# Kernel optimization log

Measured on AMD Instinct MI355X. Metric: run time of the kernel, lower is better.

The kernel has to match this reference:

```python
import jax, jax.numpy as jnp
import numpy as np

TOP_K = 2

def _expert(x, w1, w2, w3):
    return (jax.nn.silu(x @ w1.T) * (x @ w3.T)) @ w2.T

def setup_inputs() -> dict:
    key = jax.random.key(0)
    ks = jax.random.split(key, 8)
    B, L, D, F, E, S = 4, 2048, 1024, 512, 16, 1
    p = lambda k, shape: (jax.random.normal(k, shape, jnp.float32) * 0.02)
    return {
        "x": jax.random.normal(ks[0], (B, L, D), jnp.float32),
        "gate_w": p(ks[1], (E, D)),
        "expert_bias": jnp.zeros((E,), jnp.float32),
        "sw1": p(ks[2], (S, F, D)),
        "sw2": p(ks[3], (S, D, F)),
        "sw3": p(ks[4], (S, F, D)),
        "ew1": p(ks[5], (E, F, D)),
        "ew2": p(ks[6], (E, D, F)),
        "ew3": p(ks[7], (E, F, D)),
    }

def reference(x, gate_w, expert_bias, sw1, sw2, sw3, ew1, ew2, ew3):
    B, L, D = x.shape
    E = gate_w.shape[0]
    flat_x = x.reshape(-1, D)  # [T, D], T = B*L

    # Shared experts (always-on)
    shared = sum(_expert(flat_x, sw1[i], sw2[i], sw3[i]) for i in range(sw1.shape[0]))

    # Router (eval mode: no jitter noise, no bias update; expert_bias buffer added)
    logits = flat_x @ gate_w.T + expert_bias          # [T, E]
    probs = jax.nn.softmax(logits, axis=-1)
    topw, topi = jax.lax.top_k(probs, TOP_K)          # [T, k]
    topw = topw / jnp.sum(topw, axis=-1, keepdims=True)

    # Routed experts: combine weight per (token, expert); zero weight => zero contribution,
    # identical math to the masked gather/scatter in the original.
    out = jnp.zeros_like(flat_x)
    for e in range(E):  # fixed small structural loop over experts
        cw = jnp.sum(jnp.where(topi == e, topw, 0.0), axis=-1)  # [T]
        out = out + cw[:, None] * _expert(flat_x, ew1[e], ew2[e], ew3[e])

    y = (shared + out).reshape(B, L, D)
    return y, probs
```

## Files before the change

### kernel.cpp

```cpp
#include <hip/hip_runtime.h>

typedef unsigned short u16;
typedef __bf16 bf16_t;
typedef bf16_t bf16x8 __attribute__((ext_vector_type(8)));
typedef float f32x4 __attribute__((ext_vector_type(4)));

#define T_TOK 8192
#define DIM   1024
#define FF    512
#define NE    16
#define RBASE_SHARED (2 * T_TOK)
#define NROWS (RBASE_SHARED + T_TOK)
#define MAXTILES 256
#define NSEG 512

__device__ __forceinline__ u16 f2bf(float f) {
  union { float f; unsigned u; } v; v.f = f;
  unsigned r = v.u + 0x7FFFu + ((v.u >> 16) & 1u);
  return (u16)(r >> 16);
}
__device__ __forceinline__ float bf2f(u16 h) {
  union { unsigned u; float f; } v; v.u = ((unsigned)h) << 16; return v.f;
}
__device__ __forceinline__ int clampi(int v, int lo, int hi) {
  return v < lo ? lo : (v > hi ? hi : v);
}

#define GLL16(g, l) __builtin_amdgcn_global_load_lds( \
    (const __attribute__((address_space(1))) void*)(g), \
    (__attribute__((address_space(3))) void*)(l), 16, 0, 0)

#define WAIT_VM_BARRIER(n) asm volatile("s_waitcnt vmcnt(" #n ")\n\ts_barrier" ::: "memory")
#define WAIT_LGKM0()       asm volatile("s_waitcnt lgkmcnt(0)" ::: "memory")

#define SW4  131072
#define EW4  2097152
#define TOTW4 (3 * SW4 + 3 * EW4)

__global__ __launch_bounds__(256) void cvt_all_kernel(
    const float* __restrict__ sw1, const float* __restrict__ sw2,
    const float* __restrict__ sw3, const float* __restrict__ ew1,
    const float* __restrict__ ew2, const float* __restrict__ ew3,
    u16* __restrict__ sw1b, u16* __restrict__ sw2b, u16* __restrict__ sw3b,
    u16* __restrict__ ew1b, u16* __restrict__ ew2b, u16* __restrict__ ew3b) {
  int i = blockIdx.x * 256 + threadIdx.x;
  const float* s; u16* dst; int j;
  if (i < SW4)                      { s = sw1; dst = sw1b; j = i; }
  else if (i < 2 * SW4)             { s = sw2; dst = sw2b; j = i - SW4; }
  else if (i < 3 * SW4)             { s = sw3; dst = sw3b; j = i - 2 * SW4; }
  else if (i < 3 * SW4 + EW4)       { s = ew1; dst = ew1b; j = i - 3 * SW4; }
  else if (i < 3 * SW4 + 2 * EW4)   { s = ew2; dst = ew2b; j = i - (3 * SW4 + EW4); }
  else if (i < TOTW4)               { s = ew3; dst = ew3b; j = i - (3 * SW4 + 2 * EW4); }
  else return;
  float4 v = reinterpret_cast<const float4*>(s)[j];
  ushort4 o;
  o.x = f2bf(v.x); o.y = f2bf(v.y); o.z = f2bf(v.z); o.w = f2bf(v.w);
  reinterpret_cast<ushort4*>(dst)[j] = o;
}

__global__ __launch_bounds__(256) void router_kernel(
    const float* __restrict__ x, const float* __restrict__ gw,
    const float* __restrict__ ebias, float* __restrict__ probs,
    int* __restrict__ topi, float* __restrict__ topw, int* __restrict__ cnt_seg,
    u16* __restrict__ xb) {
  __shared__ int hist[16];
  int tid = threadIdx.x;
  int lane = tid & 63, w = tid >> 6;
  if (tid < 16) hist[tid] = 0;
  __syncthreads();
  const float4* gv = reinterpret_cast<const float4*>(gw);
  for (int it = 0; it < 2; ++it) {
    int t0 = blockIdx.x * 16 + (w + 4 * it) * 2;
    const float4* x0 = reinterpret_cast<const float4*>(x + (size_t)t0 * DIM);
    const float4* x1 = reinterpret_cast<const float4*>(x + (size_t)(t0 + 1) * DIM);
    float4 xa[4], xc[4];
#pragma unroll
    for (int j = 0; j < 4; ++j) { xa[j] = x0[j * 64 + lane]; xc[j] = x1[j * 64 + lane]; }
    u16* xr0 = xb + (size_t)t0 * DIM;
    u16* xr1 = xb + (size_t)(t0 + 1) * DIM;
#pragma unroll
    for (int j = 0; j < 4; ++j) {
      ushort4 o0, o1;
      o0.x = f2bf(xa[j].x); o0.y = f2bf(xa[j].y); o0.z = f2bf(xa[j].z); o0.w = f2bf(xa[j].w);
      o1.x = f2bf(xc[j].x); o1.y = f2bf(xc[j].y); o1.z = f2bf(xc[j].z); o1.w = f2bf(xc[j].w);
      reinterpret_cast<ushort4*>(xr0)[j * 64 + lane] = o0;
      reinterpret_cast<ushort4*>(xr1)[j * 64 + lane] = o1;
    }
    float p0[16], p1[16];
#pragma unroll
    for (int e = 0; e < NE; ++e) {
      float s0 = 0.f, s1 = 0.f;
#pragma unroll
      for (int j = 0; j < 4; ++j) {
        float4 g = gv[e * 256 + j * 64 + lane];
        s0 += xa[j].x * g.x + xa[j].y * g.y + xa[j].z * g.z + xa[j].w * g.w;
        s1 += xc[j].x * g.x + xc[j].y * g.y + xc[j].z * g.z + xc[j].w * g.w;
      }
#pragma unroll
      for (int d = 1; d < 64; d <<= 1) { s0 += __shfl_xor(s0, d); s1 += __shfl_xor(s1, d); }
      float b = ebias[e];
      p0[e] = s0 + b; p1[e] = s1 + b;
    }
    float m0 = p0[0], m1 = p1[0];
#pragma unroll
    for (int e = 1; e < NE; ++e) { m0 = fmaxf(m0, p0[e]); m1 = fmaxf(m1, p1[e]); }
    float sum0 = 0.f, sum1 = 0.f;
#pragma unroll
    for (int e = 0; e < NE; ++e) {
      p0[e] = __expf(p0[e] - m0); sum0 += p0[e];
      p1[e] = __expf(p1[e] - m1); sum1 += p1[e];
    }
    float inv0 = 1.f / sum0, inv1 = 1.f / sum1;
#pragma unroll
    for (int e = 0; e < NE; ++e) { p0[e] *= inv0; p1[e] *= inv1; }
    if (lane == 0) {
#pragma unroll
      for (int j = 0; j < 4; ++j)
        reinterpret_cast<float4*>(probs + (size_t)t0 * NE)[j] =
            make_float4(p0[4 * j], p0[4 * j + 1], p0[4 * j + 2], p0[4 * j + 3]);
      float b1 = -1.f, b2 = -1.f; int i1 = 0, i2 = 0;
#pragma unroll
      for (int e = 0; e < NE; ++e) {
        float pe = p0[e];
        if (pe > b1) { b2 = b1; i2 = i1; b1 = pe; i1 = e; }
        else if (pe > b2) { b2 = pe; i2 = e; }
      }
      float ws = b1 + b2;
      reinterpret_cast<int2*>(topi)[t0] = make_int2(i1, i2);
      reinterpret_cast<float2*>(topw)[t0] = make_float2(b1 / ws, b2 / ws);
      atomicAdd(&hist[i1], 1); atomicAdd(&hist[i2], 1);
    }
    if (lane == 1) {
      int t1 = t0 + 1;
#pragma unroll
      for (int j = 0; j < 4; ++j)
        reinterpret_cast<float4*>(probs + (size_t)t1 * NE)[j] =
            make_float4(p1[4 * j], p1[4 * j + 1], p1[4 * j + 2], p1[4 * j + 3]);
      float b1 = -1.f, b2 = -1.f; int i1 = 0, i2 = 0;
#pragma unroll
      for (int e = 0; e < NE; ++e) {
        float pe = p1[e];
        if (pe > b1) { b2 = b1; i2 = i1; b1 = pe; i1 = e; }
        else if (pe > b2) { b2 = pe; i2 = e; }
      }
      float ws = b1 + b2;
      reinterpret_cast<int2*>(topi)[t1] = make_int2(i1, i2);
      reinterpret_cast<float2*>(topw)[t1] = make_float2(b1 / ws, b2 / ws);
      atomicAdd(&hist[i1], 1); atomicAdd(&hist[i2], 1);
    }
  }
  __syncthreads();
  if (tid < 16) cnt_seg[blockIdx.x * 16 + tid] = hist[tid];
}

__global__ __launch_bounds__(256) void scan_kernel(
    const int* __restrict__ cnt_seg, int* __restrict__ cnt, int* __restrict__ offs,
    int* __restrict__ seg_base, int2* __restrict__ tab) {
  __shared__ int chunk_sum[16][16];
  __shared__ int chunk_base[16][16];
  __shared__ int tot[16], off_s[17];
  int tid = threadIdx.x;
  int e = tid & 15, c = tid >> 4;
  int s0 = 0;
  for (int s = 0; s < 32; ++s) s0 += cnt_seg[(c * 32 + s) * 16 + e];
  chunk_sum[c][e] = s0;
  __syncthreads();
  if (tid < 16) {
    int r = 0;
    for (int c2 = 0; c2 < 16; ++c2) { chunk_base[c2][tid] = r; r += chunk_sum[c2][tid]; }
    tot[tid] = r;
  }
  __syncthreads();
  if (tid == 0) {
    int a = 0;
    for (int i = 0; i < 16; ++i) { off_s[i] = a; offs[i] = a; cnt[i] = tot[i]; a += tot[i]; }
    off_s[16] = RBASE_SHARED; offs[16] = RBASE_SHARED;
    for (int i = 0; i < MAXTILES; ++i) tab[i] = make_int2(-1, 0);
    int loadc[8]  = {0, 0, 0, 0, 0, 0, 0, 0};
    int cursor[8] = {0, 0, 0, 0, 0, 0, 0, 0};
    for (int g = 0; g < 16; ++g) {
      int nt = (tot[g] + 127) >> 7;
      if (nt == 0) continue;
      int best = 0;
      for (int c2 = 1; c2 < 8; ++c2) if (loadc[c2] < loadc[best]) best = c2;
      loadc[best] += nt;
      int c2 = best;
      for (int ti = 0; ti < nt; ++ti) {
        while (cursor[c2] >= 32) c2 = (c2 + 1) & 7;
        tab[c2 * 32 + cursor[c2]] = make_int2(g, ti * 128);
        cursor[c2]++;
      }
    }
    for (int ti = 0; ti < 64; ++ti) {
      int c2 = ti & 7;
      while (cursor[c2] >= 32) c2 = (c2 + 1) & 7;
      tab[c2 * 32 + cursor[c2]] = make_int2(16, ti * 128);
      cursor[c2]++;
    }
  }
  __syncthreads();
  int r = off_s[e] + chunk_base[c][e];
  for (int s = 0; s < 32; ++s) {
    int seg = c * 32 + s;
    seg_base[seg * 16 + e] = r;
    r += cnt_seg[seg * 16 + e];
  }
}

__global__ __launch_bounds__(64) void scatter_kernel(
    const int* __restrict__ topi, const float* __restrict__ topw,
    const int* __restrict__ seg_base,
    int* __restrict__ idx, float* __restrict__ cwl, int* __restrict__ slotmap) {
  __shared__ int ti[16][2]; __shared__ float tw[16][2]; __shared__ int base[16];
  int b = blockIdx.x;
  int tid = threadIdx.x;
  if (tid < 16) {
    int t = b * 16 + tid;
    int2 pp = reinterpret_cast<const int2*>(topi)[t];
    ti[tid][0] = clampi(pp.x, 0, 15); ti[tid][1] = clampi(pp.y, 0, 15);
    float2 ww = reinterpret_cast<const float2*>(topw)[t];
    tw[tid][0] = ww.x; tw[tid][1] = ww.y;
    base[tid] = seg_base[b * 16 + tid];
  }
  __syncthreads();
  if (tid < 32) {
    int l = tid >> 1, s = tid & 1;
    int t = b * 16 + l;
    int e = ti[l][s];
    int rank = 0;
    for (int t2 = 0; t2 < 16; ++t2) {
      if (ti[t2][0] == e && (t2 < l || (t2 == l && 0 < s))) ++rank;
      if (ti[t2][1] == e && (t2 < l)) ++rank;
    }
    int slot = clampi(base[e] + rank, 0, NROWS - 1);
    idx[slot] = t; cwl[slot] = tw[l][s]; slotmap[t * 3 + s] = slot;
  } else if (tid < 48) {
    int l = tid - 32;
    int t = b * 16 + l;
    int sh = RBASE_SHARED + t;
    idx[sh] = t; cwl[sh] = 1.0f; slotmap[t * 3 + 2] = sh;
  }
}

__global__ __launch_bounds__(256, 2) void gemm_silu_kernel(
    const u16* __restrict__ A, const u16* __restrict__ sw1b, const u16* __restrict__ sw3b,
    const u16* __restrict__ ew1b, const u16* __restrict__ ew3b, u16* __restrict__ G,
    const int2* __restrict__ tab, const int* __restrict__ offs,
    const int* __restrict__ cnt, const int* __restrict__ gidx) {
  const int K = DIM;
  int orig = blockIdx.x;
  int xcd = orig & 7;
  int u = orig >> 3;
  int tslot = u >> 2, ny = u & 3;
  int tileid = xcd * 32 + tslot;
  int2 te = tab[tileid];
  int e = te.x;
  if (e < 0) return;
  e = clampi(e, 0, NE);
  int m0 = te.y;
  int M = (e == NE) ? T_TOK : cnt[e];
  M = clampi(M, 1, T_TOK);
  int rowbase = clampi(offs[e], 0, NROWS - 1);
  const u16* B1 = (e == NE) ? sw1b : ew1b + (size_t)e * FF * K;
  const u16* B3 = (e == NE) ? sw3b : ew3b + (size_t)e * FF * K;
  int n0 = ny * 128;

  __shared__ u16 As[3 * 4096], B1s[3 * 4096], B3s[3 * 4096];

  int tid = threadIdx.x;
  int lane = tid & 63, wv = tid >> 6;
  int srow = tid >> 2, sg = tid & 3;
  int sk0 = (sg ^ ((srow >> 1) & 3)) * 8;
  int sk1 = (sg ^ (((srow + 64) >> 1) & 3)) * 8;
  int r0 = min(m0 + srow, M - 1);
  int r1 = min(m0 + srow + 64, M - 1);
  int ga0 = clampi(gidx[clampi(rowbase + r0, 0, NROWS - 1)], 0, T_TOK - 1);
  int ga1 = clampi(gidx[clampi(rowbase + r1, 0, NROWS - 1)], 0, T_TOK - 1);
  const u16* Ap0 = A + (size_t)ga0 * K + sk0;
  const u16* Ap1 = A + (size_t)ga1 * K + sk1;
  const u16* B1p0 = B1 + (size_t)(n0 + srow) * K + sk0;
  const u16* B1p1 = B1 + (size_t)(n0 + srow + 64) * K + sk1;
  const u16* B3p0 = B3 + (size_t)(n0 + srow) * K + sk0;
  const u16* B3p1 = B3 + (size_t)(n0 + srow + 64) * K + sk1;
  int st0 = wv * 512, st1 = 2048 + wv * 512;

  int ln15 = lane & 15, qd = lane >> 4;
  int qsw = (qd ^ ((ln15 >> 1) & 3)) * 8;
  int wm = (wv >> 1) * 64, wn = (wv & 1) * 64;
  int aoff = (wm + ln15) * 32 + qsw;
  int boff = (wn + ln15) * 32 + qsw;

  f32x4 acc1[4][4] = {};
  f32x4 acc3[4][4] = {};

#pragma unroll
  for (int b = 0; b < 2; ++b) {
    const int bb = b * 4096, kb = b * 32;
    GLL16(Ap0 + kb, As + bb + st0);      GLL16(Ap1 + kb, As + bb + st1);
    GLL16(B1p0 + kb, B1s + bb + st0);    GLL16(B1p1 + kb, B1s + bb + st1);
    GLL16(B3p0 + kb, B3s + bb + st0);    GLL16(B3p1 + kb, B3s + bb + st1);
  }

#pragma unroll
  for (int t = 0; t < 30; ++t) {
    const int cur = (t % 3) * 4096;
    WAIT_VM_BARRIER(6);
    const int nxt = ((t + 2) % 3) * 4096;
    const int kt = (t + 2) * 32;
    GLL16(Ap0 + kt, As + nxt + st0);     GLL16(Ap1 + kt, As + nxt + st1);
    GLL16(B1p0 + kt, B1s + nxt + st0);   GLL16(B1p1 + kt, B1s + nxt + st1);
    GLL16(B3p0 + kt, B3s + nxt + st0);   GLL16(B3p1 + kt, B3s + nxt + st1);
    bf16x8 af[4], bx[4];
#pragma unroll
    for (int i = 0; i < 4; ++i) {
      af[i] = *reinterpret_cast<const bf16x8*>(&As[cur + aoff + i * 512]);
      bx[i] = *reinterpret_cast<const bf16x8*>(&B1s[cur + boff + i * 512]);
    }
    WAIT_LGKM0();
    __builtin_amdgcn_sched_barrier(0);
    __builtin_amdgcn_s_setprio(1);
#pragma unroll
    for (int i = 0; i < 4; ++i)
#pragma unroll
      for (int j = 0; j < 4; ++j)
        acc1[i][j] = __builtin_amdgcn_mfma_f32_16x16x32_bf16(af[i], bx[j], acc1[i][j], 0, 0, 0);
    __builtin_amdgcn_s_setprio(0);
    __builtin_amdgcn_sched_barrier(0);
#pragma unroll
    for (int i = 0; i < 4; ++i)
      bx[i] = *reinterpret_cast<const bf16x8*>(&B3s[cur + boff + i * 512]);
    WAIT_LGKM0();
    __builtin_amdgcn_sched_barrier(0);
    __builtin_amdgcn_s_setprio(1);
#pragma unroll
    for (int i = 0; i < 4; ++i)
#pragma unroll
      for (int j = 0; j < 4; ++j)
        acc3[i][j] = __builtin_amdgcn_mfma_f32_16x16x32_bf16(af[i], bx[j], acc3[i][j], 0, 0, 0);
    __builtin_amdgcn_s_setprio(0);
  }
#pragma unroll
  for (int pt = 30; pt < 32; ++pt) {
    const int cur = (pt % 3) * 4096;
    if (pt == 30) { WAIT_VM_BARRIER(6); }
    else          { WAIT_VM_BARRIER(0); }
    bf16x8 af[4], bx[4];
#pragma unroll
    for (int i = 0; i < 4; ++i) {
      af[i] = *reinterpret_cast<const bf16x8*>(&As[cur + aoff + i * 512]);
      bx[i] = *reinterpret_cast<const bf16x8*>(&B1s[cur + boff + i * 512]);
    }
    WAIT_LGKM0();
    __builtin_amdgcn_sched_barrier(0);
    __builtin_amdgcn_s_setprio(1);
#pragma unroll
    for (int i = 0; i < 4; ++i)
#pragma unroll
      for (int j = 0; j < 4; ++j)
        acc1[i][j] = __builtin_amdgcn_mfma_f32_16x16x32_bf16(af[i], bx[j], acc1[i][j], 0, 0, 0);
    __builtin_amdgcn_s_setprio(0);
    __builtin_amdgcn_sched_barrier(0);
#pragma unroll
    for (int i = 0; i < 4; ++i)
      bx[i] = *reinterpret_cast<const bf16x8*>(&B3s[cur + boff + i * 512]);
    WAIT_LGKM0();
    __builtin_amdgcn_sched_barrier(0);
    __builtin_amdgcn_s_setprio(1);
#pragma unroll
    for (int i = 0; i < 4; ++i)
#pragma unroll
      for (int j = 0; j < 4; ++j)
        acc3[i][j] = __builtin_amdgcn_mfma_f32_16x16x32_bf16(af[i], bx[j], acc3[i][j], 0, 0, 0);
    __builtin_amdgcn_s_setprio(0);
  }

  int mrem = M - m0;
#pragma unroll
  for (int i = 0; i < 4; ++i)
#pragma unroll
    for (int r2 = 0; r2 < 4; ++r2) {
      int ml = wm + i * 16 + qd * 4 + r2;
      if (ml < mrem) {
        size_t orow = (size_t)clampi(rowbase + m0 + ml, 0, NROWS - 1);
#pragma unroll
        for (int j = 0; j < 4; ++j) {
          float z1 = acc1[i][j][r2], z3 = acc3[i][j][r2];
          float g = z1 / (1.f + __expf(-z1)) * z3;
          G[orow * FF + n0 + wn + j * 16 + ln15] = f2bf(g);
        }
      }
    }
}

__global__ __launch_bounds__(256, 2) void gemm_out_kernel(
    const u16* __restrict__ Gb, const u16* __restrict__ sw2b, const u16* __restrict__ ew2b,
    u16* __restrict__ O, const int2* __restrict__ tab, const int* __restrict__ offs,
    const int* __restrict__ cnt, const float* __restrict__ cwl) {
  const int K = FF;
  int orig = blockIdx.x;
  int xcd = orig & 7;
  int u = orig >> 3;
  int tslot = u >> 3, ny = u & 7;
  int tileid = xcd * 32 + tslot;
  int2 te = tab[tileid];
  int e = te.x;
  if (e < 0) return;
  e = clampi(e, 0, NE);
  int m0 = te.y;
  int M = (e == NE) ? T_TOK : cnt[e];
  M = clampi(M, 1, T_TOK);
  int rowbase = clampi(offs[e], 0, NROWS - 1);
  const u16* B = (e == NE) ? sw2b : ew2b + (size_t)e * DIM * K;
  int n0 = ny * 128;

  __shared__ u16 As[3 * 4096], Bs[3 * 4096];

  int tid = threadIdx.x;
  int lane = tid & 63, wv = tid >> 6;
  int srow = tid >> 2, sg = tid & 3;
  int sk0 = (sg ^ ((srow >> 1) & 3)) * 8;
  int sk1 = (sg ^ (((srow + 64) >> 1) & 3)) * 8;
  int r0 = clampi(rowbase + min(m0 + srow, M - 1), 0, NROWS - 1);
  int r1 = clampi(rowbase + min(m0 + srow + 64, M - 1), 0, NROWS - 1);
  const u16* Ap0 = Gb + (size_t)r0 * K + sk0;
  const u16* Ap1 = Gb + (size_t)r1 * K + sk1;
  const u16* Bp0 = B + (size_t)(n0 + srow) * K + sk0;
  const u16* Bp1 = B + (size_t)(n0 + srow + 64) * K + sk1;
  int st0 = wv * 512, st1 = 2048 + wv * 512;

  int ln15 = lane & 15, qd = lane >> 4;
  int qsw = (qd ^ ((ln15 >> 1) & 3)) * 8;
  int wm = (wv >> 1) * 64, wn = (wv & 1) * 64;
  int aoff = (wm + ln15) * 32 + qsw;
  int boff = (wn + ln15) * 32 + qsw;

  f32x4 acc[4][4] = {};

#pragma unroll
  for (int b = 0; b < 2; ++b) {
    const int bb = b * 4096, kb = b * 32;
    GLL16(Ap0 + kb, As + bb + st0);   GLL16(Ap1 + kb, As + bb + st1);
    GLL16(Bp0 + kb, Bs + bb + st0);   GLL16(Bp1 + kb, Bs + bb + st1);
  }

#pragma unroll
  for (int t = 0; t < 14; ++t) {
    const int cur = (t % 3) * 4096;
    WAIT_VM_BARRIER(4);
    const int nxt = ((t + 2) % 3) * 4096;
    const int kt = (t + 2) * 32;
    GLL16(Ap0 + kt, As + nxt + st0);   GLL16(Ap1 + kt, As + nxt + st1);
    GLL16(Bp0 + kt, Bs + nxt + st0);   GLL16(Bp1 + kt, Bs + nxt + st1);
    bf16x8 af[4], bf[4];
#pragma unroll
    for (int i = 0; i < 4; ++i) {
      af[i] = *reinterpret_cast<const bf16x8*>(&As[cur + aoff + i * 512]);
      bf[i] = *reinterpret_cast<const bf16x8*>(&Bs[cur + boff + i * 512]);
    }
    WAIT_LGKM0();
    __builtin_amdgcn_sched_barrier(0);
    __builtin_amdgcn_s_setprio(1);
#pragma unroll
    for (int i = 0; i < 4; ++i)
#pragma unroll
      for (int j = 0; j < 4; ++j)
        acc[i][j] = __builtin_amdgcn_mfma_f32_16x16x32_bf16(af[i], bf[j], acc[i][j], 0, 0, 0);
    __builtin_amdgcn_s_setprio(0);
  }
#pragma unroll
  for (int pt = 14; pt < 16; ++pt) {
    const int cur = (pt % 3) * 4096;
    if (pt == 14) { WAIT_VM_BARRIER(4); }
    else          { WAIT_VM_BARRIER(0); }
    bf16x8 af[4], bf[4];
#pragma unroll
    for (int i = 0; i < 4; ++i) {
      af[i] = *reinterpret_cast<const bf16x8*>(&As[cur + aoff + i * 512]);
      bf[i] = *reinterpret_cast<const bf16x8*>(&Bs[cur + boff + i * 512]);
    }
    WAIT_LGKM0();
    __builtin_amdgcn_sched_barrier(0);
    __builtin_amdgcn_s_setprio(1);
#pragma unroll
    for (int i = 0; i < 4; ++i)
#pragma unroll
      for (int j = 0; j < 4; ++j)
        acc[i][j] = __builtin_amdgcn_mfma_f32_16x16x32_bf16(af[i], bf[j], acc[i][j], 0, 0, 0);
    __builtin_amdgcn_s_setprio(0);
  }

  int mrem = M - m0;
#pragma unroll
  for (int i = 0; i < 4; ++i)
#pragma unroll
    for (int r2 = 0; r2 < 4; ++r2) {
      int ml = wm + i * 16 + qd * 4 + r2;
      if (ml < mrem) {
        int slot2 = clampi(rowbase + m0 + ml, 0, NROWS - 1);
        float cw = cwl[slot2];
#pragma unroll
        for (int j = 0; j < 4; ++j)
          O[(size_t)slot2 * DIM + n0 + wn + j * 16 + ln15] = f2bf(acc[i][j][r2] * cw);
      }
    }
}

__global__ __launch_bounds__(256) void combine_kernel(
    const u16* __restrict__ O, const int* __restrict__ slotmap, float* __restrict__ y) {
  int t = blockIdx.x;
  int c = threadIdx.x;
  int s0 = clampi(slotmap[t * 3], 0, NROWS - 1);
  int s1 = clampi(slotmap[t * 3 + 1], 0, NROWS - 1);
  int s2 = clampi(slotmap[t * 3 + 2], 0, NROWS - 1);
  ushort4 a = reinterpret_cast<const ushort4*>(O + (size_t)s0 * DIM)[c];
  ushort4 b = reinterpret_cast<const ushort4*>(O + (size_t)s1 * DIM)[c];
  ushort4 d = reinterpret_cast<const ushort4*>(O + (size_t)s2 * DIM)[c];
  float4 r;
  r.x = bf2f(a.x) + bf2f(b.x) + bf2f(d.x);
  r.y = bf2f(a.y) + bf2f(b.y) + bf2f(d.y);
  r.z = bf2f(a.z) + bf2f(b.z) + bf2f(d.z);
  r.w = bf2f(a.w) + bf2f(b.w) + bf2f(d.w);
  reinterpret_cast<float4*>(y + (size_t)t * DIM)[c] = r;
}

extern "C" void kernel_launch(void* const* d_in, const int* in_sizes, int n_in,
                              void* d_out, int out_size, void* d_ws, size_t ws_size,
                              hipStream_t stream) {
  const float* x     = (const float*)d_in[0];
  const float* gw    = (const float*)d_in[1];
  const float* ebias = (const float*)d_in[2];
  const float* sw1   = (const float*)d_in[3];
  const float* sw2   = (const float*)d_in[4];
  const float* sw3   = (const float*)d_in[5];
  const float* ew1   = (const float*)d_in[6];
  const float* ew2   = (const float*)d_in[7];
  const float* ew3   = (const float*)d_in[8];
  float* y = (float*)d_out;
  float* probs = y + (size_t)T_TOK * DIM;

  char* ws = (char*)d_ws;
  size_t o = 0;
  auto alloc = [&](size_t bytes) -> char* {
    char* p = ws + o;
    o = (o + bytes + 255) & ~(size_t)255;
    return p;
  };
  u16* G    = (u16*)alloc((size_t)NROWS * FF * 2);
  u16* sw1b = (u16*)alloc((size_t)FF * DIM * 2);
  u16* sw2b = (u16*)alloc((size_t)FF * DIM * 2);
  u16* sw3b = (u16*)alloc((size_t)FF * DIM * 2);
  u16* ew2b = (u16*)alloc((size_t)NE * FF * DIM * 2);
  char* aliasBase = alloc((size_t)NROWS * DIM * 2);
  u16* xb   = (u16*)aliasBase;
  u16* ew1b = (u16*)(aliasBase + (size_t)T_TOK * DIM * 2);
  u16* ew3b = (u16*)(aliasBase + (size_t)T_TOK * DIM * 2 + (size_t)NE * FF * DIM * 2);
  u16* O    = (u16*)aliasBase;
  int*   topi    = (int*)alloc(T_TOK * 2 * 4);
  float* topw    = (float*)alloc(T_TOK * 2 * 4);
  int*   idx     = (int*)alloc(NROWS * 4);
  float* cwl     = (float*)alloc(NROWS * 4);
  int*   slotmap = (int*)alloc(T_TOK * 3 * 4);
  int2*  tab     = (int2*)alloc(MAXTILES * 8);
  int*   cnt_seg = (int*)alloc(NSEG * 16 * 4);
  int*   seg_base= (int*)alloc(NSEG * 16 * 4);
  int*   cnt     = (int*)alloc(256);
  int*   offs    = (int*)alloc(256);

  router_kernel<<<NSEG, 256, 0, stream>>>(x, gw, ebias, probs, topi, topw, cnt_seg, xb);
  scan_kernel<<<1, 256, 0, stream>>>(cnt_seg, cnt, offs, seg_base, tab);
  scatter_kernel<<<NSEG, 64, 0, stream>>>(topi, topw, seg_base, idx, cwl, slotmap);
  cvt_all_kernel<<<TOTW4 / 256, 256, 0, stream>>>(sw1, sw2, sw3, ew1, ew2, ew3,
                                                  sw1b, sw2b, sw3b, ew1b, ew2b, ew3b);

  gemm_silu_kernel<<<1024, 256, 0, stream>>>(
      xb, sw1b, sw3b, ew1b, ew3b, G, tab, offs, cnt, idx);
  gemm_out_kernel<<<2048, 256, 0, stream>>>(
      G, sw2b, ew2b, O, tab, offs, cnt, cwl);
  combine_kernel<<<T_TOK, 256, 0, stream>>>(O, slotmap, y);
}
```

Measured before the change: 379.3 us.

## Make expert GEMMs persistent per-XCD loops over tile tables

Both grouped GEMM kernels become persistent: 512 blocks loop over per-XCD tile lists, bounded by a new per-XCD tile count that the scan kernel writes. This removes launches of blocks that would only exit early on empty table entries, and keeps each block's work on its XCD. The silu GEMM also issues the B3 LDS fragment reads together with the B1 reads and waits with lgkmcnt(4), so the B3 loads overlap the first MFMA batch. The cost is more live registers, plus a full vmcnt(0) barrier between tiles that drains the pipeline at every tile boundary.

```diff
diff --git a/kernel.cpp b/kernel.cpp
--- a/kernel.cpp
+++ b/kernel.cpp
@@ -32,6 +32,7 @@
 
 #define WAIT_VM_BARRIER(n) asm volatile("s_waitcnt vmcnt(" #n ")\n\ts_barrier" ::: "memory")
 #define WAIT_LGKM0()       asm volatile("s_waitcnt lgkmcnt(0)" ::: "memory")
+#define WAIT_LGKM4()       asm volatile("s_waitcnt lgkmcnt(4)" ::: "memory")
 
 #define SW4  131072
 #define EW4  2097152
@@ -155,7 +156,7 @@
 
 __global__ __launch_bounds__(256) void scan_kernel(
     const int* __restrict__ cnt_seg, int* __restrict__ cnt, int* __restrict__ offs,
-    int* __restrict__ seg_base, int2* __restrict__ tab) {
+    int* __restrict__ seg_base, int2* __restrict__ tab, int* __restrict__ ntile) {
   __shared__ int chunk_sum[16][16];
   __shared__ int chunk_base[16][16];
   __shared__ int tot[16], off_s[17];
@@ -197,6 +198,7 @@
       tab[c2 * 32 + cursor[c2]] = make_int2(16, ti * 128);
       cursor[c2]++;
     }
+    for (int c2 = 0; c2 < 8; ++c2) ntile[c2] = cursor[c2];
   }
   __syncthreads();
   int r = off_s[e] + chunk_base[c][e];
@@ -246,24 +248,13 @@
     const u16* __restrict__ A, const u16* __restrict__ sw1b, const u16* __restrict__ sw3b,
     const u16* __restrict__ ew1b, const u16* __restrict__ ew3b, u16* __restrict__ G,
     const int2* __restrict__ tab, const int* __restrict__ offs,
-    const int* __restrict__ cnt, const int* __restrict__ gidx) {
+    const int* __restrict__ cnt, const int* __restrict__ gidx,
+    const int* __restrict__ ntile) {
   const int K = DIM;
-  int orig = blockIdx.x;
-  int xcd = orig & 7;
-  int u = orig >> 3;
-  int tslot = u >> 2, ny = u & 3;
-  int tileid = xcd * 32 + tslot;
-  int2 te = tab[tileid];
-  int e = te.x;
-  if (e < 0) return;
-  e = clampi(e, 0, NE);
-  int m0 = te.y;
-  int M = (e == NE) ? T_TOK : cnt[e];
-  M = clampi(M, 1, T_TOK);
-  int rowbase = clampi(offs[e], 0, NROWS - 1);
-  const u16* B1 = (e == NE) ? sw1b : ew1b + (size_t)e * FF * K;
-  const u16* B3 = (e == NE) ? sw3b : ew3b + (size_t)e * FF * K;
-  int n0 = ny * 128;
+  int bid = blockIdx.x;
+  int xcd = bid & 7;
+  int q = bid >> 3;
+  int Nit = clampi(ntile[xcd], 0, 32) * 4;
 
   __shared__ u16 As[3 * 4096], B1s[3 * 4096], B3s[3 * 4096];
 
@@ -272,146 +263,150 @@
   int srow = tid >> 2, sg = tid & 3;
   int sk0 = (sg ^ ((srow >> 1) & 3)) * 8;
   int sk1 = (sg ^ (((srow + 64) >> 1) & 3)) * 8;
-  int r0 = min(m0 + srow, M - 1);
-  int r1 = min(m0 + srow + 64, M - 1);
-  int ga0 = clampi(gidx[clampi(rowbase + r0, 0, NROWS - 1)], 0, T_TOK - 1);
-  int ga1 = clampi(gidx[clampi(rowbase + r1, 0, NROWS - 1)], 0, T_TOK - 1);
-  const u16* Ap0 = A + (size_t)ga0 * K + sk0;
-  const u16* Ap1 = A + (size_t)ga1 * K + sk1;
-  const u16* B1p0 = B1 + (size_t)(n0 + srow) * K + sk0;
-  const u16* B1p1 = B1 + (size_t)(n0 + srow + 64) * K + sk1;
-  const u16* B3p0 = B3 + (size_t)(n0 + srow) * K + sk0;
-  const u16* B3p1 = B3 + (size_t)(n0 + srow + 64) * K + sk1;
   int st0 = wv * 512, st1 = 2048 + wv * 512;
-
   int ln15 = lane & 15, qd = lane >> 4;
   int qsw = (qd ^ ((ln15 >> 1) & 3)) * 8;
   int wm = (wv >> 1) * 64, wn = (wv & 1) * 64;
   int aoff = (wm + ln15) * 32 + qsw;
   int boff = (wn + ln15) * 32 + qsw;
 
-  f32x4 acc1[4][4] = {};
-  f32x4 acc3[4][4] = {};
-
-#pragma unroll
-  for (int b = 0; b < 2; ++b) {
-    const int bb = b * 4096, kb = b * 32;
-    GLL16(Ap0 + kb, As + bb + st0);      GLL16(Ap1 + kb, As + bb + st1);
-    GLL16(B1p0 + kb, B1s + bb + st0);    GLL16(B1p1 + kb, B1s + bb + st1);
-    GLL16(B3p0 + kb, B3s + bb + st0);    GLL16(B3p1 + kb, B3s + bb + st1);
-  }
-
-#pragma unroll
-  for (int t = 0; t < 30; ++t) {
-    const int cur = (t % 3) * 4096;
-    WAIT_VM_BARRIER(6);
-    const int nxt = ((t + 2) % 3) * 4096;
-    const int kt = (t + 2) * 32;
-    GLL16(Ap0 + kt, As + nxt + st0);     GLL16(Ap1 + kt, As + nxt + st1);
-    GLL16(B1p0 + kt, B1s + nxt + st0);   GLL16(B1p1 + kt, B1s + nxt + st1);
-    GLL16(B3p0 + kt, B3s + nxt + st0);   GLL16(B3p1 + kt, B3s + nxt + st1);
-    bf16x8 af[4], bx[4];
-#pragma unroll
-    for (int i = 0; i < 4; ++i) {
-      af[i] = *reinterpret_cast<const bf16x8*>(&As[cur + aoff + i * 512]);
-      bx[i] = *reinterpret_cast<const bf16x8*>(&B1s[cur + boff + i * 512]);
-    }
-    WAIT_LGKM0();
-    __builtin_amdgcn_sched_barrier(0);
-    __builtin_amdgcn_s_setprio(1);
+  for (int it = q; it < Nit; it += 64) {
+    WAIT_VM_BARRIER(0);
+    int tslot = it >> 2, ny = it & 3;
+    int2 te = tab[xcd * 32 + tslot];
+    int e = te.x;
+    if (e < 0) continue;
+    e = clampi(e, 0, NE);
+    int m0 = te.y;
+    int M = (e == NE) ? T_TOK : cnt[e];
+    M = clampi(M, 1, T_TOK);
+    int rowbase = clampi(offs[e], 0, NROWS - 1);
+    const u16* B1 = (e == NE) ? sw1b : ew1b + (size_t)e * FF * K;
+    const u16* B3 = (e == NE) ? sw3b : ew3b + (size_t)e * FF * K;
+    int n0 = ny * 128;
+
+    int r0 = min(m0 + srow, M - 1);
+    int r1 = min(m0 + srow + 64, M - 1);
+    int ga0 = clampi(gidx[clampi(rowbase + r0, 0, NROWS - 1)], 0, T_TOK - 1);
+    int ga1 = clampi(gidx[clampi(rowbase + r1, 0, NROWS - 1)], 0, T_TOK - 1);
+    const u16* Ap0 = A + (size_t)ga0 * K + sk0;
+    const u16* Ap1 = A + (size_t)ga1 * K + sk1;
+    const u16* B1p0 = B1 + (size_t)(n0 + srow) * K + sk0;
+    const u16* B1p1 = B1 + (size_t)(n0 + srow + 64) * K + sk1;
+    const u16* B3p0 = B3 + (size_t)(n0 + srow) * K + sk0;
+    const u16* B3p1 = B3 + (size_t)(n0 + srow + 64) * K + sk1;
+
+    f32x4 acc1[4][4] = {};
+    f32x4 acc3[4][4] = {};
+
+#pragma unroll
+    for (int b = 0; b < 2; ++b) {
+      const int bb = b * 4096, kb = b * 32;
+      GLL16(Ap0 + kb, As + bb + st0);      GLL16(Ap1 + kb, As + bb + st1);
+      GLL16(B1p0 + kb, B1s + bb + st0);    GLL16(B1p1 + kb, B1s + bb + st1);
+      GLL16(B3p0 + kb, B3s + bb + st0);    GLL16(B3p1 + kb, B3s + bb + st1);
+    }
+
+#pragma unroll
+    for (int t = 0; t < 30; ++t) {
+      const int cur = (t % 3) * 4096;
+      WAIT_VM_BARRIER(6);
+      const int nxt = ((t + 2) % 3) * 4096;
+      const int kt = (t + 2) * 32;
+      GLL16(Ap0 + kt, As + nxt + st0);     GLL16(Ap1 + kt, As + nxt + st1);
+      GLL16(B1p0 + kt, B1s + nxt + st0);   GLL16(B1p1 + kt, B1s + nxt + st1);
+      GLL16(B3p0 + kt, B3s + nxt + st0);   GLL16(B3p1 + kt, B3s + nxt + st1);
+      bf16x8 af[4], b1f[4], b3f[4];
+#pragma unroll
+      for (int i = 0; i < 4; ++i) {
+        af[i]  = *reinterpret_cast<const bf16x8*>(&As[cur + aoff + i * 512]);
+        b1f[i] = *reinterpret_cast<const bf16x8*>(&B1s[cur + boff + i * 512]);
+      }
+#pragma unroll
+      for (int i = 0; i < 4; ++i)
+        b3f[i] = *reinterpret_cast<const bf16x8*>(&B3s[cur + boff + i * 512]);
+      WAIT_LGKM4();
+      __builtin_amdgcn_sched_barrier(0);
+      __builtin_amdgcn_s_setprio(1);
+#pragma unroll
+      for (int i = 0; i < 4; ++i)
+#pragma unroll
+        for (int j = 0; j < 4; ++j)
+          acc1[i][j] = __builtin_amdgcn_mfma_f32_16x16x32_bf16(af[i], b1f[j], acc1[i][j], 0, 0, 0);
+      __builtin_amdgcn_s_setprio(0);
+      WAIT_LGKM0();
+      __builtin_amdgcn_sched_barrier(0);
+      __builtin_amdgcn_s_setprio(1);
+#pragma unroll
+      for (int i = 0; i < 4; ++i)
+#pragma unroll
+        for (int j = 0; j < 4; ++j)
+          acc3[i][j] = __builtin_amdgcn_mfma_f32_16x16x32_bf16(af[i], b3f[j], acc3[i][j], 0, 0, 0);
+      __builtin_amdgcn_s_setprio(0);
+    }
+#pragma unroll
+    for (int pt = 30; pt < 32; ++pt) {
+      const int cur = (pt % 3) * 4096;
+      if (pt == 30) { WAIT_VM_BARRIER(6); }
+      else          { WAIT_VM_BARRIER(0); }
+      bf16x8 af[4], b1f[4], b3f[4];
+#pragma unroll
+      for (int i = 0; i < 4; ++i) {
+        af[i]  = *reinterpret_cast<const bf16x8*>(&As[cur + aoff + i * 512]);
+        b1f[i] = *reinterpret_cast<const bf16x8*>(&B1s[cur + boff + i * 512]);
+      }
+#pragma unroll
+      for (int i = 0; i < 4; ++i)
+        b3f[i] = *reinterpret_cast<const bf16x8*>(&B3s[cur + boff + i * 512]);
+      WAIT_LGKM4();
+      __builtin_amdgcn_sched_barrier(0);
+      __builtin_amdgcn_s_setprio(1);
+#pragma unroll
+      for (int i = 0; i < 4; ++i)
+#pragma unroll
+        for (int j = 0; j < 4; ++j)
+          acc1[i][j] = __builtin_amdgcn_mfma_f32_16x16x32_bf16(af[i], b1f[j], acc1[i][j], 0, 0, 0);
+      __builtin_amdgcn_s_setprio(0);
+      WAIT_LGKM0();
+      __builtin_amdgcn_sched_barrier(0);
+      __builtin_amdgcn_s_setprio(1);
+#pragma unroll
+      for (int i = 0; i < 4; ++i)
+#pragma unroll
+        for (int j = 0; j < 4; ++j)
+          acc3[i][j] = __builtin_amdgcn_mfma_f32_16x16x32_bf16(af[i], b3f[j], acc3[i][j], 0, 0, 0);
+      __builtin_amdgcn_s_setprio(0);
+    }
+
+    int mrem = M - m0;
 #pragma unroll
     for (int i = 0; i < 4; ++i)
 #pragma unroll
-      for (int j = 0; j < 4; ++j)
-        acc1[i][j] = __builtin_amdgcn_mfma_f32_16x16x32_bf16(af[i], bx[j], acc1[i][j], 0, 0, 0);
-    __builtin_amdgcn_s_setprio(0);
-    __builtin_amdgcn_sched_barrier(0);
-#pragma unroll
-    for (int i = 0; i < 4; ++i)
-      bx[i] = *reinterpret_cast<const bf16x8*>(&B3s[cur + boff + i * 512]);
-    WAIT_LGKM0();
-    __builtin_amdgcn_sched_barrier(0);
-    __builtin_amdgcn_s_setprio(1);
-#pragma unroll
-    for (int i = 0; i < 4; ++i)
-#pragma unroll
-      for (int j = 0; j < 4; ++j)
-        acc3[i][j] = __builtin_amdgcn_mfma_f32_16x16x32_bf16(af[i], bx[j], acc3[i][j], 0, 0, 0);
-    __builtin_amdgcn_s_setprio(0);
-  }
-#pragma unroll
-  for (int pt = 30; pt < 32; ++pt) {
-    const int cur = (pt % 3) * 4096;
-    if (pt == 30) { WAIT_VM_BARRIER(6); }
-    else          { WAIT_VM_BARRIER(0); }
-    bf16x8 af[4], bx[4];
-#pragma unroll
-    for (int i = 0; i < 4; ++i) {
-      af[i] = *reinterpret_cast<const bf16x8*>(&As[cur + aoff + i * 512]);
-      bx[i] = *reinterpret_cast<const bf16x8*>(&B1s[cur + boff + i * 512]);
-    }
-    WAIT_LGKM0();
-    __builtin_amdgcn_sched_barrier(0);
-    __builtin_amdgcn_s_setprio(1);
-#pragma unroll
-    for (int i = 0; i < 4; ++i)
-#pragma unroll
-      for (int j = 0; j < 4; ++j)
-        acc1[i][j] = __builtin_amdgcn_mfma_f32_16x16x32_bf16(af[i], bx[j], acc1[i][j], 0, 0, 0);
-    __builtin_amdgcn_s_setprio(0);
-    __builtin_amdgcn_sched_barrier(0);
-#pragma unroll
-    for (int i = 0; i < 4; ++i)
-      bx[i] = *reinterpret_cast<const bf16x8*>(&B3s[cur + boff + i * 512]);
-    WAIT_LGKM0();
-    __builtin_amdgcn_sched_barrier(0);
-    __builtin_amdgcn_s_setprio(1);
-#pragma unroll
-    for (int i = 0; i < 4; ++i)
-#pragma unroll
-      for (int j = 0; j < 4; ++j)
-        acc3[i][j] = __builtin_amdgcn_mfma_f32_16x16x32_bf16(af[i], bx[j], acc3[i][j], 0, 0, 0);
-    __builtin_amdgcn_s_setprio(0);
-  }
-
-  int mrem = M - m0;
-#pragma unroll
-  for (int i = 0; i < 4; ++i)
-#pragma unroll
-    for (int r2 = 0; r2 < 4; ++r2) {
-      int ml = wm + i * 16 + qd * 4 + r2;
-      if (ml < mrem) {
-        size_t orow = (size_t)clampi(rowbase + m0 + ml, 0, NROWS - 1);
-#pragma unroll
-        for (int j = 0; j < 4; ++j) {
-          float z1 = acc1[i][j][r2], z3 = acc3[i][j][r2];
-          float g = z1 / (1.f + __expf(-z1)) * z3;
-          G[orow * FF + n0 + wn + j * 16 + ln15] = f2bf(g);
+      for (int r2 = 0; r2 < 4; ++r2) {
+        int ml = wm + i * 16 + qd * 4 + r2;
+        if (ml < mrem) {
+          size_t orow = (size_t)clampi(rowbase + m0 + ml, 0, NROWS - 1);
+#pragma unroll
+          for (int j = 0; j < 4; ++j) {
+            float z1 = acc1[i][j][r2], z3 = acc3[i][j][r2];
+            float g = z1 / (1.f + __expf(-z1)) * z3;
+            G[orow * FF + n0 + wn + j * 16 + ln15] = f2bf(g);
+          }
         }
       }
-    }
+  }
 }
 
 __global__ __launch_bounds__(256, 2) void gemm_out_kernel(
     const u16* __restrict__ Gb, const u16* __restrict__ sw2b, const u16* __restrict__ ew2b,
     u16* __restrict__ O, const int2* __restrict__ tab, const int* __restrict__ offs,
-    const int* __restrict__ cnt, const float* __restrict__ cwl) {
+    const int* __restrict__ cnt, const float* __restrict__ cwl,
+    const int* __restrict__ ntile) {
   const int K = FF;
-  int orig = blockIdx.x;
-  int xcd = orig & 7;
-  int u = orig >> 3;
-  int tslot = u >> 3, ny = u & 7;
-  int tileid = xcd * 32 + tslot;
-  int2 te = tab[tileid];
-  int e = te.x;
-  if (e < 0) return;
-  e = clampi(e, 0, NE);
-  int m0 = te.y;
-  int M = (e == NE) ? T_TOK : cnt[e];
-  M = clampi(M, 1, T_TOK);
-  int rowbase = clampi(offs[e], 0, NROWS - 1);
-  const u16* B = (e == NE) ? sw2b : ew2b + (size_t)e * DIM * K;
-  int n0 = ny * 128;
+  int bid = blockIdx.x;
+  int xcd = bid & 7;
+  int q = bid >> 3;
+  int Nit = clampi(ntile[xcd], 0, 32) * 8;
 
   __shared__ u16 As[3 * 4096], Bs[3 * 4096];
 
@@ -420,89 +415,104 @@
   int srow = tid >> 2, sg = tid & 3;
   int sk0 = (sg ^ ((srow >> 1) & 3)) * 8;
   int sk1 = (sg ^ (((srow + 64) >> 1) & 3)) * 8;
-  int r0 = clampi(rowbase + min(m0 + srow, M - 1), 0, NROWS - 1);
-  int r1 = clampi(rowbase + min(m0 + srow + 64, M - 1), 0, NROWS - 1);
-  const u16* Ap0 = Gb + (size_t)r0 * K + sk0;
-  const u16* Ap1 = Gb + (size_t)r1 * K + sk1;
-  const u16* Bp0 = B + (size_t)(n0 + srow) * K + sk0;
-  const u16* Bp1 = B + (size_t)(n0 + srow + 64) * K + sk1;
   int st0 = wv * 512, st1 = 2048 + wv * 512;
-
   int ln15 = lane & 15, qd = lane >> 4;
   int qsw = (qd ^ ((ln15 >> 1) & 3)) * 8;
   int wm = (wv >> 1) * 64, wn = (wv & 1) * 64;
   int aoff = (wm + ln15) * 32 + qsw;
   int boff = (wn + ln15) * 32 + qsw;
 
-  f32x4 acc[4][4] = {};
-
-#pragma unroll
-  for (int b = 0; b < 2; ++b) {
-    const int bb = b * 4096, kb = b * 32;
-    GLL16(Ap0 + kb, As + bb + st0);   GLL16(Ap1 + kb, As + bb + st1);
-    GLL16(Bp0 + kb, Bs + bb + st0);   GLL16(Bp1 + kb, Bs + bb + st1);
-  }
-
-#pragma unroll
-  for (int t = 0; t < 14; ++t) {
-    const int cur = (t % 3) * 4096;
-    WAIT_VM_BARRIER(4);
-    const int nxt = ((t + 2) % 3) * 4096;
-    const int kt = (t + 2) * 32;
-    GLL16(Ap0 + kt, As + nxt + st0);   GLL16(Ap1 + kt, As + nxt + st1);
-    GLL16(Bp0 + kt, Bs + nxt + st0);   GLL16(Bp1 + kt, Bs + nxt + st1);
-    bf16x8 af[4], bf[4];
-#pragma unroll
-    for (int i = 0; i < 4; ++i) {
-      af[i] = *reinterpret_cast<const bf16x8*>(&As[cur + aoff + i * 512]);
-      bf[i] = *reinterpret_cast<const bf16x8*>(&Bs[cur + boff + i * 512]);
-    }
-    WAIT_LGKM0();
-    __builtin_amdgcn_sched_barrier(0);
-    __builtin_amdgcn_s_setprio(1);
+  for (int it = q; it < Nit; it += 64) {
+    WAIT_VM_BARRIER(0);
+    int tslot = it >> 3, ny = it & 7;
+    int2 te = tab[xcd * 32 + tslot];
+    int e = te.x;
+    if (e < 0) continue;
+    e = clampi(e, 0, NE);
+    int m0 = te.y;
+    int M = (e == NE) ? T_TOK : cnt[e];
+    M = clampi(M, 1, T_TOK);
+    int rowbase = clampi(offs[e], 0, NROWS - 1);
+    const u16* B = (e == NE) ? sw2b : ew2b + (size_t)e * DIM * K;
+    int n0 = ny * 128;
+
+    int r0 = clampi(rowbase + min(m0 + srow, M - 1), 0, NROWS - 1);
+    int r1 = clampi(rowbase + min(m0 + srow + 64, M - 1), 0, NROWS - 1);
+    const u16* Ap0 = Gb + (size_t)r0 * K + sk0;
+    const u16* Ap1 = Gb + (size_t)r1 * K + sk1;
+    const u16* Bp0 = B + (size_t)(n0 + srow) * K + sk0;
+    const u16* Bp1 = B + (size_t)(n0 + srow + 64) * K + sk1;
+
+    f32x4 acc[4][4] = {};
+
+#pragma unroll
+    for (int b = 0; b < 2; ++b) {
+      const int bb = b * 4096, kb = b * 32;
+      GLL16(Ap0 + kb, As + bb + st0);   GLL16(Ap1 + kb, As + bb + st1);
+      GLL16(Bp0 + kb, Bs + bb + st0);   GLL16(Bp1 + kb, Bs + bb + st1);
+    }
+
+#pragma unroll
+    for (int t = 0; t < 14; ++t) {
+      const int cur = (t % 3) * 4096;
+      WAIT_VM_BARRIER(4);
+      const int nxt = ((t + 2) % 3) * 4096;
+      const int kt = (t + 2) * 32;
+      GLL16(Ap0 + kt, As + nxt + st0);   GLL16(Ap1 + kt, As + nxt + st1);
+      GLL16(Bp0 + kt, Bs + nxt + st0);   GLL16(Bp1 + kt, Bs + nxt + st1);
+      bf16x8 af[4], bf[4];
+#pragma unroll
+      for (int i = 0; i < 4; ++i) {
+        af[i] = *reinterpret_cast<const bf16x8*>(&As[cur + aoff + i * 512]);
+        bf[i] = *reinterpret_cast<const bf16x8*>(&Bs[cur + boff + i * 512]);
+      }
+      WAIT_LGKM0();
+      __builtin_amdgcn_sched_barrier(0);
+      __builtin_amdgcn_s_setprio(1);
+#pragma unroll
+      for (int i = 0; i < 4; ++i)
+#pragma unroll
+        for (int j = 0; j < 4; ++j)
+          acc[i][j] = __builtin_amdgcn_mfma_f32_16x16x32_bf16(af[i], bf[j], acc[i][j], 0, 0, 0);
+      __builtin_amdgcn_s_setprio(0);
+    }
+#pragma unroll
+    for (int pt = 14; pt < 16; ++pt) {
+      const int cur = (pt % 3) * 4096;
+      if (pt == 14) { WAIT_VM_BARRIER(4); }
+      else          { WAIT_VM_BARRIER(0); }
+      bf16x8 af[4], bf[4];
+#pragma unroll
+      for (int i = 0; i < 4; ++i) {
+        af[i] = *reinterpret_cast<const bf16x8*>(&As[cur + aoff + i * 512]);
+        bf[i] = *reinterpret_cast<const bf16x8*>(&Bs[cur + boff + i * 512]);
+      }
+      WAIT_LGKM0();
+      __builtin_amdgcn_sched_barrier(0);
+      __builtin_amdgcn_s_setprio(1);
+#pragma unroll
+      for (int i = 0; i < 4; ++i)
+#pragma unroll
+        for (int j = 0; j < 4; ++j)
+          acc[i][j] = __builtin_amdgcn_mfma_f32_16x16x32_bf16(af[i], bf[j], acc[i][j], 0, 0, 0);
+      __builtin_amdgcn_s_setprio(0);
+    }
+
+    int mrem = M - m0;
 #pragma unroll
     for (int i = 0; i < 4; ++i)
 #pragma unroll
-      for (int j = 0; j < 4; ++j)
-        acc[i][j] = __builtin_amdgcn_mfma_f32_16x16x32_bf16(af[i], bf[j], acc[i][j], 0, 0, 0);
-    __builtin_amdgcn_s_setprio(0);
-  }
-#pragma unroll
-  for (int pt = 14; pt < 16; ++pt) {
-    const int cur = (pt % 3) * 4096;
-    if (pt == 14) { WAIT_VM_BARRIER(4); }
-    else          { WAIT_VM_BARRIER(0); }
-    bf16x8 af[4], bf[4];
-#pragma unroll
-    for (int i = 0; i < 4; ++i) {
-      af[i] = *reinterpret_cast<const bf16x8*>(&As[cur + aoff + i * 512]);
-      bf[i] = *reinterpret_cast<const bf16x8*>(&Bs[cur + boff + i * 512]);
-    }
-    WAIT_LGKM0();
-    __builtin_amdgcn_sched_barrier(0);
-    __builtin_amdgcn_s_setprio(1);
-#pragma unroll
-    for (int i = 0; i < 4; ++i)
-#pragma unroll
-      for (int j = 0; j < 4; ++j)
-        acc[i][j] = __builtin_amdgcn_mfma_f32_16x16x32_bf16(af[i], bf[j], acc[i][j], 0, 0, 0);
-    __builtin_amdgcn_s_setprio(0);
-  }
-
-  int mrem = M - m0;
-#pragma unroll
-  for (int i = 0; i < 4; ++i)
-#pragma unroll
-    for (int r2 = 0; r2 < 4; ++r2) {
-      int ml = wm + i * 16 + qd * 4 + r2;
-      if (ml < mrem) {
-        int slot2 = clampi(rowbase + m0 + ml, 0, NROWS - 1);
-        float cw = cwl[slot2];
-#pragma unroll
-        for (int j = 0; j < 4; ++j)
-          O[(size_t)slot2 * DIM + n0 + wn + j * 16 + ln15] = f2bf(acc[i][j][r2] * cw);
-      }
-    }
+      for (int r2 = 0; r2 < 4; ++r2) {
+        int ml = wm + i * 16 + qd * 4 + r2;
+        if (ml < mrem) {
+          int slot2 = clampi(rowbase + m0 + ml, 0, NROWS - 1);
+          float cw = cwl[slot2];
+#pragma unroll
+          for (int j = 0; j < 4; ++j)
+            O[(size_t)slot2 * DIM + n0 + wn + j * 16 + ln15] = f2bf(acc[i][j][r2] * cw);
+        }
+      }
+  }
 }
 
 __global__ __launch_bounds__(256) void combine_kernel(
@@ -565,16 +575,17 @@
   int*   seg_base= (int*)alloc(NSEG * 16 * 4);
   int*   cnt     = (int*)alloc(256);
   int*   offs    = (int*)alloc(256);
+  int*   ntile   = (int*)alloc(64);
 
   router_kernel<<<NSEG, 256, 0, stream>>>(x, gw, ebias, probs, topi, topw, cnt_seg, xb);
-  scan_kernel<<<1, 256, 0, stream>>>(cnt_seg, cnt, offs, seg_base, tab);
+  scan_kernel<<<1, 256, 0, stream>>>(cnt_seg, cnt, offs, seg_base, tab, ntile);
   scatter_kernel<<<NSEG, 64, 0, stream>>>(topi, topw, seg_base, idx, cwl, slotmap);
   cvt_all_kernel<<<TOTW4 / 256, 256, 0, stream>>>(sw1, sw2, sw3, ew1, ew2, ew3,
                                                   sw1b, sw2b, sw3b, ew1b, ew2b, ew3b);
 
-  gemm_silu_kernel<<<1024, 256, 0, stream>>>(
-      xb, sw1b, sw3b, ew1b, ew3b, G, tab, offs, cnt, idx);
-  gemm_out_kernel<<<2048, 256, 0, stream>>>(
-      G, sw2b, ew2b, O, tab, offs, cnt, cwl);
+  gemm_silu_kernel<<<512, 256, 0, stream>>>(
+      xb, sw1b, sw3b, ew1b, ew3b, G, tab, offs, cnt, idx, ntile);
+  gemm_out_kernel<<<512, 256, 0, stream>>>(
+      G, sw2b, ew2b, O, tab, offs, cnt, cwl, ntile);
   combine_kernel<<<T_TOK, 256, 0, stream>>>(O, slotmap, y);
 }
```

Result: slower. 394.9 us (+4.1%).
